# Optimization experiments

Hardware: AMD Instinct MI355X
Metric: run time of the kernel (lower is better)

Reference implementation:

```python
import jax, jax.numpy as jnp
import numpy as np

EMB, HEAD = 2048, 128

def setup_inputs() -> dict:
    key = jax.random.key(0)
    ks = jax.random.split(key, 7)
    x = jax.random.normal(ks[0], (4, 4096, EMB), dtype=jnp.float32)
    s = 1.0 / np.sqrt(EMB)
    wK = jax.random.normal(ks[1], (EMB, HEAD), dtype=jnp.float32) * s
    bK = jax.random.normal(ks[2], (HEAD,), dtype=jnp.float32) * 0.01
    wQ = jax.random.normal(ks[3], (EMB, HEAD), dtype=jnp.float32) * s
    bQ = jax.random.normal(ks[4], (HEAD,), dtype=jnp.float32) * 0.01
    wV = jax.random.normal(ks[5], (EMB, HEAD), dtype=jnp.float32) * s
    bV = jax.random.normal(ks[6], (HEAD,), dtype=jnp.float32) * 0.01
    return {"x": x, "wK": wK, "bK": bK, "wQ": wQ, "bQ": bQ, "wV": wV, "bV": bV}

def reference(x, wK, bK, wQ, bQ, wV, bV):
    B, S, E = x.shape
    K = x @ wK + bK                      # [B,S,H]
    Q = x @ wQ + bQ
    V = x @ wV + bV
    scale = 1.0 / jnp.sqrt(jnp.float32(HEAD))
    att = jnp.einsum('bqh,bkh->bqk', Q, K) * scale   # [B,S,S]
    causal = jnp.tril(jnp.ones((S, S), dtype=bool))
    att = jnp.where(causal, att, -jnp.inf)
    att = jax.nn.softmax(att, axis=-1)
    return jnp.einsum('bqk,bkh->bqh', att, V)        # [B,S,H]
```

## Files before the change

### kernel.cpp

```cpp
#include <hip/hip_runtime.h>
#include <hip/hip_bf16.h>
#include <math.h>

#define SEQ  4096
#define BATCH 4
#define EMBD 2048
#define HDIM 128

#define SCALE_LOG2E 0.12753102721944556f

typedef __bf16 bf16x8 __attribute__((ext_vector_type(8)));
typedef __bf16 bf16x4 __attribute__((ext_vector_type(4)));
typedef float  f32x4  __attribute__((ext_vector_type(4)));

__device__ __forceinline__ bf16x8 ldfrag(const __bf16* p) {
    return *(const bf16x8*)p;
}

__device__ __forceinline__ void gl_lds16(const __bf16* g, __bf16* l) {
    __builtin_amdgcn_global_load_lds(
        (const __attribute__((address_space(1))) void*)g,
        (__attribute__((address_space(3))) void*)l, 16, 0, 0);
}

__global__ __launch_bounds__(256)
void cvt_x(const float* __restrict__ x, __bf16* __restrict__ xb) {
    size_t idx = (size_t)(blockIdx.x * 256 + threadIdx.x) * 8;
    float4 v0 = *(const float4*)(x + idx);
    float4 v1 = *(const float4*)(x + idx + 4);
    bf16x8 o = { (__bf16)v0.x, (__bf16)v0.y, (__bf16)v0.z, (__bf16)v0.w,
                 (__bf16)v1.x, (__bf16)v1.y, (__bf16)v1.z, (__bf16)v1.w };
    *(bf16x8*)(xb + idx) = o;
}

__global__ __launch_bounds__(256)
void cvt_w(const float* __restrict__ wQ, const float* __restrict__ wK,
           const float* __restrict__ wV, __bf16* __restrict__ wt) {
    const float* w = (blockIdx.z == 0) ? wQ : (blockIdx.z == 1) ? wK : wV;
    __bf16* dst = wt + (size_t)blockIdx.z * HDIM * EMBD;
    int k0 = blockIdx.x * 32;
    int n0 = blockIdx.y * 32;
    __shared__ float t[32][33];
    {
        int r  = threadIdx.x >> 3;
        int c4 = (threadIdx.x & 7) * 4;
        float4 v = *(const float4*)(w + (size_t)(k0 + r) * HDIM + n0 + c4);
        t[r][c4 + 0] = v.x; t[r][c4 + 1] = v.y;
        t[r][c4 + 2] = v.z; t[r][c4 + 3] = v.w;
    }
    __syncthreads();
    {
        int n  = threadIdx.x >> 3;
        int k4 = (threadIdx.x & 7) * 4;
        bf16x4 o = { (__bf16)t[k4 + 0][n], (__bf16)t[k4 + 1][n],
                     (__bf16)t[k4 + 2][n], (__bf16)t[k4 + 3][n] };
        *(bf16x4*)(dst + (size_t)(n0 + n) * EMBD + k0 + k4) = o;
    }
}

__global__ __launch_bounds__(256, 3)
void proj(const __bf16* __restrict__ xb,
          const __bf16* __restrict__ wt,
          __bf16* __restrict__ pout) {
    const int mat  = blockIdx.y;
    const int z    = blockIdx.z;
    const int m0   = blockIdx.x * 128;
    const int kb   = z * (EMBD / 2);
    const int wv   = threadIdx.x >> 6;
    const int lane = threadIdx.x & 63;
    const int ln   = lane & 15;
    const int quad = lane >> 4;
    const int r8   = lane >> 3;
    const int c8   = lane & 7;

    __shared__ __bf16 lA[128 * 64];
    __shared__ __bf16 lB[128 * 64];

    const __bf16* wtm = wt + (size_t)mat * (HDIM * EMBD);
    const __bf16* gaS = xb  + (size_t)(m0 + wv * 32 + r8) * EMBD + kb + (c8 ^ r8) * 8;
    const __bf16* gbS = wtm + (size_t)(wv * 32 + r8) * EMBD + kb + (c8 ^ r8) * 8;
    __bf16* laD = lA + (wv * 32) * 64;
    __bf16* lbD = lB + (wv * 32) * 64;

    const int wm0 = (wv >> 1) * 64;
    const int wn0 = (wv & 1) * 64;

    const f32x4 fzero = {0.f, 0.f, 0.f, 0.f};
    f32x4 acc[4][4];
#pragma unroll
    for (int i = 0; i < 4; i++)
#pragma unroll
        for (int j = 0; j < 4; j++) acc[i][j] = fzero;

    for (int k0 = 0; k0 < EMBD / 2; k0 += 64) {
#pragma unroll
        for (int i = 0; i < 4; i++) {
            gl_lds16(gaS + (size_t)i * 8 * EMBD + k0, laD + i * 8 * 64);
            gl_lds16(gbS + (size_t)i * 8 * EMBD + k0, lbD + i * 8 * 64);
        }
        __syncthreads();
#pragma unroll
        for (int kk = 0; kk < 2; kk++) {
            bf16x8 a[4], bb[4];
#pragma unroll
            for (int i = 0; i < 4; i++)
                a[i] = ldfrag(lA + (wm0 + i * 16 + ln) * 64 +
                              (((quad + 4 * kk) ^ (ln & 7)) * 8));
#pragma unroll
            for (int j = 0; j < 4; j++)
                bb[j] = ldfrag(lB + (wn0 + j * 16 + ln) * 64 +
                               (((quad + 4 * kk) ^ (ln & 7)) * 8));
#pragma unroll
            for (int i = 0; i < 4; i++)
#pragma unroll
                for (int j = 0; j < 4; j++)
                    acc[i][j] = __builtin_amdgcn_mfma_f32_16x16x32_bf16(
                        a[i], bb[j], acc[i][j], 0, 0, 0);
        }
        __syncthreads();
    }

    __bf16* pp = pout + (size_t)(mat * 2 + z) * 16384 * 128;
#pragma unroll
    for (int j = 0; j < 4; j++) {
        int col = wn0 + j * 16 + ln;
#pragma unroll
        for (int i = 0; i < 4; i++) {
            int rowb = m0 + wm0 + i * 16 + quad * 4;
#pragma unroll
            for (int r = 0; r < 4; r++)
                pp[(size_t)(rowb + r) * 128 + col] = (__bf16)acc[i][j][r];
        }
    }
}

__global__ __launch_bounds__(256)
void qkv_fin(const __bf16* __restrict__ pout,
             const float* __restrict__ bQ, const float* __restrict__ bK,
             const float* __restrict__ bV,
             __bf16* __restrict__ qws, __bf16* __restrict__ kws,
             __bf16* __restrict__ vtws) {
    const int mat = blockIdx.y;
    const int r0  = blockIdx.x * 16;
    const int t   = threadIdx.x;
    const int rl  = t >> 4;
    const int cc  = (t & 15) * 8;
    const float* bias = (mat == 0) ? bQ : (mat == 1) ? bK : bV;

    bf16x8 p0 = *(const bf16x8*)(pout +
        ((size_t)(mat * 2 + 0) * 16384 + r0 + rl) * 128 + cc);
    bf16x8 p1 = *(const bf16x8*)(pout +
        ((size_t)(mat * 2 + 1) * 16384 + r0 + rl) * 128 + cc);
    float s[8];
#pragma unroll
    for (int i = 0; i < 8; i++)
        s[i] = (float)p0[i] + (float)p1[i] + bias[cc + i];

    if (mat < 2) {
        __bf16* dst = (mat == 0) ? qws : kws;
        bf16x8 o;
#pragma unroll
        for (int i = 0; i < 8; i++) o[i] = (__bf16)s[i];
        *(bf16x8*)(dst + (size_t)(r0 + rl) * 128 + cc) = o;
    } else {
        __shared__ float sm[16][132];
#pragma unroll
        for (int i = 0; i < 8; i++) sm[rl][cc + i] = s[i];
        __syncthreads();
        int col = t >> 1, sg = (t & 1) * 8;
        int bb = r0 >> 12, s0 = r0 & (SEQ - 1);
        bf16x8 o;
#pragma unroll
        for (int i = 0; i < 8; i++) o[i] = (__bf16)sm[sg + i][col];
        *(bf16x8*)(vtws + ((size_t)bb * HDIM + col) * SEQ + s0 + sg) = o;
    }
}

__global__ __launch_bounds__(256, 2)
void attn(const __bf16* __restrict__ qws, const __bf16* __restrict__ kws,
          const __bf16* __restrict__ vtws,
          float* __restrict__ Opart, float* __restrict__ Lpart) {
    const int blk = blockIdx.x;
    const int b   = (blk & 7) >> 1;
    int wi = ((blk >> 3) << 1) | (blk & 1);
    wi = 287 - wi;
    int a = (int)((sqrtf((float)wi + 1.0f) - 1.0f) * 0.5f);
    while (4 * (a + 1) * (a + 2) <= wi) a++;
    while (a > 0 && 4 * a * (a + 1) > wi) a--;
    const int rem = wi - 4 * a * (a + 1);
    const int qt  = a * 8 + rem / (a + 1);
    const int c   = rem - (rem / (a + 1)) * (a + 1);
    const int q0  = qt * 64;
    const int kt0 = c * 8;
    const int kt1 = (kt0 + 8 < qt + 1) ? (kt0 + 8) : (qt + 1);
    const int slot = b * 288 + wi;

    const int wv   = threadIdx.x >> 6;
    const int lane = threadIdx.x & 63;
    const int ln   = lane & 15;
    const int quad = lane >> 4;

    __shared__ __bf16 lK[2][64 * 128];
    __shared__ __bf16 lV[2][128 * 64];
    __shared__ __bf16 lP[4][16 * 72];

    const __bf16* kws_b = kws + (size_t)b * SEQ * HDIM;
    const __bf16* vt_b  = vtws + (size_t)b * HDIM * SEQ;

    const __bf16* qbase =
        qws + ((size_t)(b * SEQ) + q0 + wv * 16 + ln) * HDIM + quad * 8;
    bf16x8 qf[4];
#pragma unroll
    for (int kk = 0; kk < 4; kk++) qf[kk] = ldfrag(qbase + kk * 32);

    const f32x4 fzero = {0.f, 0.f, 0.f, 0.f};
    float lrun[4];
    f32x4 oacc[8];
#pragma unroll
    for (int r = 0; r < 4; r++) lrun[r] = 0.f;
#pragma unroll
    for (int j = 0; j < 8; j++) oacc[j] = fzero;

    const int krow_i = lane >> 4, kslot = lane & 15;
    const int vrow_i = lane >> 3, vslot = lane & 7;

    auto stageK = [&](int k0, int buf) {
#pragma unroll
        for (int i = 0; i < 4; i++) {
            int row = wv * 16 + i * 4 + krow_i;
            const __bf16* src = kws_b + (size_t)(k0 + row) * HDIM +
                                ((kslot ^ (row & 7)) * 8);
            gl_lds16(src, &lK[buf][(wv * 16 + i * 4) * 128]);
        }
    };
    auto stageV = [&](int k0, int buf) {
#pragma unroll
        for (int i = 0; i < 4; i++) {
            int row = wv * 32 + i * 8 + vrow_i;
            const __bf16* src = vt_b + (size_t)row * SEQ + k0 +
                                ((vslot ^ (row & 7)) * 8);
            gl_lds16(src, &lV[buf][(wv * 32 + i * 8) * 64]);
        }
    };

    stageK(kt0 * 64, 0);
    stageV(kt0 * 64, 0);

    for (int kt = kt0; kt < kt1; kt++) {
        __syncthreads();
        const int cur = (kt - kt0) & 1;
        if (kt + 1 < kt1) {
            stageK((kt + 1) * 64, cur ^ 1);
            stageV((kt + 1) * 64, cur ^ 1);
        }

        f32x4 sacc[4];
#pragma unroll
        for (int j = 0; j < 4; j++) sacc[j] = fzero;
        const __bf16* Kb = lK[cur];
#pragma unroll
        for (int j = 0; j < 4; j++) {
#pragma unroll
            for (int kk = 0; kk < 4; kk++) {
                bf16x8 kf = ldfrag(Kb + (j * 16 + ln) * 128 +
                                   (((quad + 4 * kk) ^ (ln & 7)) * 8));
                sacc[j] = __builtin_amdgcn_mfma_f32_16x16x32_bf16(
                    qf[kk], kf, sacc[j], 0, 0, 0);
            }
        }

        const bool diag = (kt == qt);
#pragma unroll
        for (int j = 0; j < 4; j++) {
#pragma unroll
            for (int r = 0; r < 4; r++) {
                float p = exp2f(sacc[j][r] * SCALE_LOG2E);
                if (diag) {
                    int col = kt * 64 + j * 16 + ln;
                    int row = q0 + wv * 16 + quad * 4 + r;
                    if (col > row) p = 0.f;
                }
                lrun[r] += p;
                lP[wv][(quad * 4 + r) * 72 + j * 16 + ln] = (__bf16)p;
            }
        }

        __builtin_amdgcn_s_waitcnt(0xc07f);
        bf16x8 af0 = ldfrag(&lP[wv][ln * 72 + quad * 8]);
        bf16x8 af1 = ldfrag(&lP[wv][ln * 72 + 32 + quad * 8]);

        const __bf16* Vb = lV[cur];
#pragma unroll
        for (int j = 0; j < 8; j++) {
            bf16x8 v0 = ldfrag(Vb + (j * 16 + ln) * 64 +
                               ((quad ^ (ln & 7)) * 8));
            bf16x8 v1 = ldfrag(Vb + (j * 16 + ln) * 64 +
                               (((quad + 4) ^ (ln & 7)) * 8));
            oacc[j] = __builtin_amdgcn_mfma_f32_16x16x32_bf16(
                af0, v0, oacc[j], 0, 0, 0);
            oacc[j] = __builtin_amdgcn_mfma_f32_16x16x32_bf16(
                af1, v1, oacc[j], 0, 0, 0);
        }
    }

#pragma unroll
    for (int r = 0; r < 4; r++) {
#pragma unroll
        for (int off = 8; off >= 1; off >>= 1)
            lrun[r] += __shfl_xor(lrun[r], off);
    }
    if (ln == 0) {
#pragma unroll
        for (int r = 0; r < 4; r++)
            Lpart[(size_t)slot * 64 + wv * 16 + quad * 4 + r] = lrun[r];
    }
    float* Ob = Opart + (size_t)slot * 8192;
#pragma unroll
    for (int r = 0; r < 4; r++) {
        int row = wv * 16 + quad * 4 + r;
#pragma unroll
        for (int j = 0; j < 8; j++)
            Ob[(size_t)row * 128 + j * 16 + ln] = oacc[j][r];
    }
}

__global__ __launch_bounds__(256)
void attn_fin(const float* __restrict__ Opart, const float* __restrict__ Lpart,
              float* __restrict__ out) {
    const int b  = blockIdx.x >> 6;
    const int qt = blockIdx.x & 63;
    const int a  = qt >> 3;
    const int nch = a + 1;
    const int base = b * 288 + 4 * a * (a + 1) + (qt & 7) * (a + 1);
    const int row = threadIdx.x >> 2;
    const int c0  = (threadIdx.x & 3) * 32;

    float l = 0.f;
    f32x4 o[8];
#pragma unroll
    for (int i = 0; i < 8; i++) o[i] = {0.f, 0.f, 0.f, 0.f};
    for (int ch = 0; ch < nch; ch++) {
        const f32x4* Op = (const f32x4*)(Opart + (size_t)(base + ch) * 8192 +
                                         (size_t)row * 128 + c0);
        l += Lpart[(size_t)(base + ch) * 64 + row];
#pragma unroll
        for (int i = 0; i < 8; i++) o[i] += Op[i];
    }
    float inv = 1.f / l;
    f32x4* orow = (f32x4*)(out + ((size_t)(b * SEQ) + qt * 64 + row) * HDIM + c0);
#pragma unroll
    for (int i = 0; i < 8; i++) orow[i] = o[i] * inv;
}

extern "C" void kernel_launch(void* const* d_in, const int* in_sizes, int n_in,
                              void* d_out, int out_size, void* d_ws,
                              size_t ws_size, hipStream_t stream) {
    const float* x  = (const float*)d_in[0];
    const float* wK = (const float*)d_in[1];
    const float* bK = (const float*)d_in[2];
    const float* wQ = (const float*)d_in[3];
    const float* bQ = (const float*)d_in[4];
    const float* wV = (const float*)d_in[5];
    const float* bV = (const float*)d_in[6];
    float* out = (float*)d_out;

    __bf16* xb   = (__bf16*)d_ws;
    __bf16* wt   = xb + (size_t)BATCH * SEQ * EMBD;
    __bf16* qws  = wt + (size_t)3 * HDIM * EMBD;
    __bf16* kws  = qws + (size_t)BATCH * SEQ * HDIM;
    __bf16* vtws = kws + (size_t)BATCH * SEQ * HDIM;
    __bf16* pout = vtws + (size_t)BATCH * SEQ * HDIM;
    float* Opart = (float*)d_ws;
    float* Lpart = Opart + (size_t)1152 * 8192;

    hipLaunchKernelGGL(cvt_w, dim3(EMBD / 32, HDIM / 32, 3), dim3(256), 0,
                       stream, wQ, wK, wV, wt);
    hipLaunchKernelGGL(cvt_x, dim3((size_t)BATCH * SEQ * EMBD / (8 * 256)),
                       dim3(256), 0, stream, x, xb);
    hipLaunchKernelGGL(proj, dim3(SEQ * BATCH / 128, 3, 2), dim3(256), 0,
                       stream, xb, wt, pout);
    hipLaunchKernelGGL(qkv_fin, dim3(SEQ * BATCH / 16, 3), dim3(256), 0,
                       stream, pout, bQ, bK, bV, qws, kws, vtws);
    hipLaunchKernelGGL(attn, dim3(1152), dim3(256), 0, stream,
                       qws, kws, vtws, Opart, Lpart);
    hipLaunchKernelGGL(attn_fin, dim3(256), dim3(256), 0, stream,
                       Opart, Lpart, out);
}
```

Measured before the change: 307.8 us.

## Switch to 32x32x16 MFMA and enlarge attention query tiles to 128 rows

Replaces the 16x16x32 MFMA tiles in the projection and attention kernels with 32x32x16 MFMA, which gives each wave a 32-row tile and more reuse per fragment load. The attention work split moves from 64-row query tiles in 8-key-tile chunks (1152 blocks) to 128-row query tiles in 16-key-tile chunks (320 blocks). Half the waves are skipped on the last diagonal key tile. Larger accumulators raise register pressure. Far fewer blocks may underfill the GPU, and the partial-sum workspace layout changes to match.

```diff
diff --git a/kernel.cpp b/kernel.cpp
--- a/kernel.cpp
+++ b/kernel.cpp
@@ -1,6 +1,5 @@
 #include <hip/hip_runtime.h>
 #include <hip/hip_bf16.h>
-#include <math.h>
 
 #define SEQ  4096
 #define BATCH 4
@@ -12,6 +11,7 @@
 typedef __bf16 bf16x8 __attribute__((ext_vector_type(8)));
 typedef __bf16 bf16x4 __attribute__((ext_vector_type(4)));
 typedef float  f32x4  __attribute__((ext_vector_type(4)));
+typedef float  f32x16 __attribute__((ext_vector_type(16)));
 
 __device__ __forceinline__ bf16x8 ldfrag(const __bf16* p) {
     return *(const bf16x8*)p;
@@ -68,8 +68,8 @@
     const int kb   = z * (EMBD / 2);
     const int wv   = threadIdx.x >> 6;
     const int lane = threadIdx.x & 63;
-    const int ln   = lane & 15;
-    const int quad = lane >> 4;
+    const int l31  = lane & 31;
+    const int h    = lane >> 5;
     const int r8   = lane >> 3;
     const int c8   = lane & 7;
 
@@ -85,12 +85,13 @@
     const int wm0 = (wv >> 1) * 64;
     const int wn0 = (wv & 1) * 64;
 
-    const f32x4 fzero = {0.f, 0.f, 0.f, 0.f};
-    f32x4 acc[4][4];
-#pragma unroll
-    for (int i = 0; i < 4; i++)
-#pragma unroll
-        for (int j = 0; j < 4; j++) acc[i][j] = fzero;
+    f32x16 acc[2][2];
+#pragma unroll
+    for (int i = 0; i < 2; i++)
+#pragma unroll
+        for (int j = 0; j < 2; j++)
+#pragma unroll
+            for (int e = 0; e < 16; e++) acc[i][j][e] = 0.f;
 
     for (int k0 = 0; k0 < EMBD / 2; k0 += 64) {
 #pragma unroll
@@ -100,21 +101,24 @@
         }
         __syncthreads();
 #pragma unroll
-        for (int kk = 0; kk < 2; kk++) {
-            bf16x8 a[4], bb[4];
-#pragma unroll
-            for (int i = 0; i < 4; i++)
-                a[i] = ldfrag(lA + (wm0 + i * 16 + ln) * 64 +
-                              (((quad + 4 * kk) ^ (ln & 7)) * 8));
-#pragma unroll
-            for (int j = 0; j < 4; j++)
-                bb[j] = ldfrag(lB + (wn0 + j * 16 + ln) * 64 +
-                               (((quad + 4 * kk) ^ (ln & 7)) * 8));
-#pragma unroll
-            for (int i = 0; i < 4; i++)
-#pragma unroll
-                for (int j = 0; j < 4; j++)
-                    acc[i][j] = __builtin_amdgcn_mfma_f32_16x16x32_bf16(
+        for (int kk = 0; kk < 4; kk++) {
+            const int ch = kk * 2 + h;
+            bf16x8 a[2], bb[2];
+#pragma unroll
+            for (int i = 0; i < 2; i++) {
+                int row = wm0 + i * 32 + l31;
+                a[i] = ldfrag(lA + row * 64 + ((ch ^ (row & 7)) * 8));
+            }
+#pragma unroll
+            for (int j = 0; j < 2; j++) {
+                int row = wn0 + j * 32 + l31;
+                bb[j] = ldfrag(lB + row * 64 + ((ch ^ (row & 7)) * 8));
+            }
+#pragma unroll
+            for (int i = 0; i < 2; i++)
+#pragma unroll
+                for (int j = 0; j < 2; j++)
+                    acc[i][j] = __builtin_amdgcn_mfma_f32_32x32x16_bf16(
                         a[i], bb[j], acc[i][j], 0, 0, 0);
         }
         __syncthreads();
@@ -122,16 +126,16 @@
 
     __bf16* pp = pout + (size_t)(mat * 2 + z) * 16384 * 128;
 #pragma unroll
-    for (int j = 0; j < 4; j++) {
-        int col = wn0 + j * 16 + ln;
-#pragma unroll
-        for (int i = 0; i < 4; i++) {
-            int rowb = m0 + wm0 + i * 16 + quad * 4;
-#pragma unroll
-            for (int r = 0; r < 4; r++)
-                pp[(size_t)(rowb + r) * 128 + col] = (__bf16)acc[i][j][r];
-        }
-    }
+    for (int i = 0; i < 2; i++)
+#pragma unroll
+        for (int j = 0; j < 2; j++) {
+            int n = wn0 + j * 32 + l31;
+#pragma unroll
+            for (int reg = 0; reg < 16; reg++) {
+                int m = m0 + wm0 + i * 32 + (reg & 3) + 8 * (reg >> 2) + 4 * h;
+                pp[(size_t)m * 128 + n] = (__bf16)acc[i][j][reg];
+            }
+        }
 }
 
 __global__ __launch_bounds__(256)
@@ -176,50 +180,50 @@
     }
 }
 
-__global__ __launch_bounds__(256, 2)
+__global__ __launch_bounds__(256)
 void attn(const __bf16* __restrict__ qws, const __bf16* __restrict__ kws,
           const __bf16* __restrict__ vtws,
           float* __restrict__ Opart, float* __restrict__ Lpart) {
     const int blk = blockIdx.x;
     const int b   = (blk & 7) >> 1;
     int wi = ((blk >> 3) << 1) | (blk & 1);
-    wi = 287 - wi;
-    int a = (int)((sqrtf((float)wi + 1.0f) - 1.0f) * 0.5f);
-    while (4 * (a + 1) * (a + 2) <= wi) a++;
-    while (a > 0 && 4 * a * (a + 1) > wi) a--;
+    wi = 79 - wi;
+    const int a   = (wi < 8) ? 0 : (wi < 24) ? 1 : (wi < 48) ? 2 : 3;
     const int rem = wi - 4 * a * (a + 1);
     const int qt  = a * 8 + rem / (a + 1);
     const int c   = rem - (rem / (a + 1)) * (a + 1);
-    const int q0  = qt * 64;
-    const int kt0 = c * 8;
-    const int kt1 = (kt0 + 8 < qt + 1) ? (kt0 + 8) : (qt + 1);
-    const int slot = b * 288 + wi;
+    const int q0  = qt * 128;
+    const int kt0 = c * 16;
+    const int ktN = 2 * qt + 2;
+    const int kt1 = (kt0 + 16 < ktN) ? (kt0 + 16) : ktN;
+    const int slot = b * 80 + wi;
 
     const int wv   = threadIdx.x >> 6;
     const int lane = threadIdx.x & 63;
-    const int ln   = lane & 15;
-    const int quad = lane >> 4;
-
-    __shared__ __bf16 lK[2][64 * 128];
-    __shared__ __bf16 lV[2][128 * 64];
-    __shared__ __bf16 lP[4][16 * 72];
+    const int l31  = lane & 31;
+    const int h    = lane >> 5;
+
+    __shared__ __align__(16) __bf16 lK[2][64 * 128];
+    __shared__ __align__(16) __bf16 lV[2][128 * 64];
+    __shared__ __align__(16) __bf16 lP[4][32 * 72];
 
     const __bf16* kws_b = kws + (size_t)b * SEQ * HDIM;
     const __bf16* vt_b  = vtws + (size_t)b * HDIM * SEQ;
 
     const __bf16* qbase =
-        qws + ((size_t)(b * SEQ) + q0 + wv * 16 + ln) * HDIM + quad * 8;
-    bf16x8 qf[4];
-#pragma unroll
-    for (int kk = 0; kk < 4; kk++) qf[kk] = ldfrag(qbase + kk * 32);
-
-    const f32x4 fzero = {0.f, 0.f, 0.f, 0.f};
-    float lrun[4];
-    f32x4 oacc[8];
-#pragma unroll
-    for (int r = 0; r < 4; r++) lrun[r] = 0.f;
-#pragma unroll
-    for (int j = 0; j < 8; j++) oacc[j] = fzero;
+        qws + ((size_t)(b * SEQ) + q0 + wv * 32 + l31) * HDIM + h * 8;
+    bf16x8 qf[8];
+#pragma unroll
+    for (int ks = 0; ks < 8; ks++) qf[ks] = ldfrag(qbase + ks * 16);
+
+    float lrun[16];
+#pragma unroll
+    for (int e = 0; e < 16; e++) lrun[e] = 0.f;
+    f32x16 oacc[4];
+#pragma unroll
+    for (int jj = 0; jj < 4; jj++)
+#pragma unroll
+        for (int e = 0; e < 16; e++) oacc[jj][e] = 0.f;
 
     const int krow_i = lane >> 4, kslot = lane & 15;
     const int vrow_i = lane >> 3, vslot = lane & 7;
@@ -254,102 +258,113 @@
             stageV((kt + 1) * 64, cur ^ 1);
         }
 
-        f32x4 sacc[4];
-#pragma unroll
-        for (int j = 0; j < 4; j++) sacc[j] = fzero;
-        const __bf16* Kb = lK[cur];
-#pragma unroll
-        for (int j = 0; j < 4; j++) {
-#pragma unroll
-            for (int kk = 0; kk < 4; kk++) {
-                bf16x8 kf = ldfrag(Kb + (j * 16 + ln) * 128 +
-                                   (((quad + 4 * kk) ^ (ln & 7)) * 8));
-                sacc[j] = __builtin_amdgcn_mfma_f32_16x16x32_bf16(
-                    qf[kk], kf, sacc[j], 0, 0, 0);
-            }
-        }
-
-        const bool diag = (kt == qt);
-#pragma unroll
-        for (int j = 0; j < 4; j++) {
-#pragma unroll
-            for (int r = 0; r < 4; r++) {
-                float p = exp2f(sacc[j][r] * SCALE_LOG2E);
-                if (diag) {
-                    int col = kt * 64 + j * 16 + ln;
-                    int row = q0 + wv * 16 + quad * 4 + r;
-                    if (col > row) p = 0.f;
+        const bool active = !(kt == 2 * qt + 1 && wv < 2);
+        if (active) {
+            f32x16 sacc[2];
+#pragma unroll
+            for (int j = 0; j < 2; j++)
+#pragma unroll
+                for (int e = 0; e < 16; e++) sacc[j][e] = 0.f;
+            const __bf16* Kb = lK[cur];
+#pragma unroll
+            for (int ks = 0; ks < 8; ks++) {
+                const int c16 = ks * 2 + h;
+#pragma unroll
+                for (int j = 0; j < 2; j++) {
+                    int row = j * 32 + l31;
+                    bf16x8 kf = ldfrag(Kb + row * 128 +
+                                       ((c16 ^ (row & 7)) * 8));
+                    sacc[j] = __builtin_amdgcn_mfma_f32_32x32x16_bf16(
+                        qf[ks], kf, sacc[j], 0, 0, 0);
                 }
-                lrun[r] += p;
-                lP[wv][(quad * 4 + r) * 72 + j * 16 + ln] = (__bf16)p;
-            }
-        }
-
-        __builtin_amdgcn_s_waitcnt(0xc07f);
-        bf16x8 af0 = ldfrag(&lP[wv][ln * 72 + quad * 8]);
-        bf16x8 af1 = ldfrag(&lP[wv][ln * 72 + 32 + quad * 8]);
-
-        const __bf16* Vb = lV[cur];
-#pragma unroll
-        for (int j = 0; j < 8; j++) {
-            bf16x8 v0 = ldfrag(Vb + (j * 16 + ln) * 64 +
-                               ((quad ^ (ln & 7)) * 8));
-            bf16x8 v1 = ldfrag(Vb + (j * 16 + ln) * 64 +
-                               (((quad + 4) ^ (ln & 7)) * 8));
-            oacc[j] = __builtin_amdgcn_mfma_f32_16x16x32_bf16(
-                af0, v0, oacc[j], 0, 0, 0);
-            oacc[j] = __builtin_amdgcn_mfma_f32_16x16x32_bf16(
-                af1, v1, oacc[j], 0, 0, 0);
-        }
-    }
-
-#pragma unroll
-    for (int r = 0; r < 4; r++) {
-#pragma unroll
-        for (int off = 8; off >= 1; off >>= 1)
-            lrun[r] += __shfl_xor(lrun[r], off);
-    }
-    if (ln == 0) {
-#pragma unroll
-        for (int r = 0; r < 4; r++)
-            Lpart[(size_t)slot * 64 + wv * 16 + quad * 4 + r] = lrun[r];
-    }
-    float* Ob = Opart + (size_t)slot * 8192;
-#pragma unroll
-    for (int r = 0; r < 4; r++) {
-        int row = wv * 16 + quad * 4 + r;
-#pragma unroll
-        for (int j = 0; j < 8; j++)
-            Ob[(size_t)row * 128 + j * 16 + ln] = oacc[j][r];
+            }
+
+            const bool maskt = (kt >= 2 * qt);
+#pragma unroll
+            for (int j = 0; j < 2; j++) {
+#pragma unroll
+                for (int reg = 0; reg < 16; reg++) {
+                    int rl = (reg & 3) + 8 * (reg >> 2) + 4 * h;
+                    float p = exp2f(sacc[j][reg] * SCALE_LOG2E);
+                    if (maskt) {
+                        int col = kt * 64 + j * 32 + l31;
+                        int row = q0 + wv * 32 + rl;
+                        if (col > row) p = 0.f;
+                    }
+                    lrun[reg] += (j == 0) ? p : p;
+                    lP[wv][rl * 72 + j * 32 + l31] = (__bf16)p;
+                }
+            }
+
+            __builtin_amdgcn_s_waitcnt(0xc07f);
+            const __bf16* Vb = lV[cur];
+#pragma unroll
+            for (int ks2 = 0; ks2 < 4; ks2++) {
+                bf16x8 af = ldfrag(&lP[wv][l31 * 72 + ks2 * 16 + h * 8]);
+                const int ch = ks2 * 2 + h;
+#pragma unroll
+                for (int jj = 0; jj < 4; jj++) {
+                    int row = jj * 32 + l31;
+                    bf16x8 vf = ldfrag(Vb + row * 64 +
+                                       ((ch ^ (row & 7)) * 8));
+                    oacc[jj] = __builtin_amdgcn_mfma_f32_32x32x16_bf16(
+                        af, vf, oacc[jj], 0, 0, 0);
+                }
+            }
+        }
+    }
+
+#pragma unroll
+    for (int reg = 0; reg < 16; reg++) {
+#pragma unroll
+        for (int off = 16; off >= 1; off >>= 1)
+            lrun[reg] += __shfl_xor(lrun[reg], off);
+    }
+    if (l31 == 0) {
+#pragma unroll
+        for (int reg = 0; reg < 16; reg++) {
+            int row = wv * 32 + (reg & 3) + 8 * (reg >> 2) + 4 * h;
+            Lpart[(size_t)slot * 128 + row] = lrun[reg];
+        }
+    }
+    float* Ob = Opart + (size_t)slot * 16384;
+#pragma unroll
+    for (int jj = 0; jj < 4; jj++) {
+        int col = jj * 32 + l31;
+#pragma unroll
+        for (int reg = 0; reg < 16; reg++) {
+            int row = wv * 32 + (reg & 3) + 8 * (reg >> 2) + 4 * h;
+            Ob[(size_t)row * 128 + col] = oacc[jj][reg];
+        }
     }
 }
 
 __global__ __launch_bounds__(256)
 void attn_fin(const float* __restrict__ Opart, const float* __restrict__ Lpart,
               float* __restrict__ out) {
-    const int b  = blockIdx.x >> 6;
-    const int qt = blockIdx.x & 63;
+    const int b  = blockIdx.x >> 5;
+    const int qt = blockIdx.x & 31;
     const int a  = qt >> 3;
     const int nch = a + 1;
-    const int base = b * 288 + 4 * a * (a + 1) + (qt & 7) * (a + 1);
-    const int row = threadIdx.x >> 2;
-    const int c0  = (threadIdx.x & 3) * 32;
+    const int base = b * 80 + 4 * a * (a + 1) + (qt & 7) * (a + 1);
+    const int row = threadIdx.x >> 1;
+    const int c0  = (threadIdx.x & 1) * 64;
 
     float l = 0.f;
-    f32x4 o[8];
-#pragma unroll
-    for (int i = 0; i < 8; i++) o[i] = {0.f, 0.f, 0.f, 0.f};
+    f32x4 o[16];
+#pragma unroll
+    for (int i = 0; i < 16; i++) o[i] = {0.f, 0.f, 0.f, 0.f};
     for (int ch = 0; ch < nch; ch++) {
-        const f32x4* Op = (const f32x4*)(Opart + (size_t)(base + ch) * 8192 +
+        const f32x4* Op = (const f32x4*)(Opart + (size_t)(base + ch) * 16384 +
                                          (size_t)row * 128 + c0);
-        l += Lpart[(size_t)(base + ch) * 64 + row];
-#pragma unroll
-        for (int i = 0; i < 8; i++) o[i] += Op[i];
+        l += Lpart[(size_t)(base + ch) * 128 + row];
+#pragma unroll
+        for (int i = 0; i < 16; i++) o[i] += Op[i];
     }
     float inv = 1.f / l;
-    f32x4* orow = (f32x4*)(out + ((size_t)(b * SEQ) + qt * 64 + row) * HDIM + c0);
-#pragma unroll
-    for (int i = 0; i < 8; i++) orow[i] = o[i] * inv;
+    f32x4* orow = (f32x4*)(out + ((size_t)(b * SEQ) + qt * 128 + row) * HDIM + c0);
+#pragma unroll
+    for (int i = 0; i < 16; i++) orow[i] = o[i] * inv;
 }
 
 extern "C" void kernel_launch(void* const* d_in, const int* in_sizes, int n_in,
@@ -371,7 +386,7 @@
     __bf16* vtws = kws + (size_t)BATCH * SEQ * HDIM;
     __bf16* pout = vtws + (size_t)BATCH * SEQ * HDIM;
     float* Opart = (float*)d_ws;
-    float* Lpart = Opart + (size_t)1152 * 8192;
+    float* Lpart = Opart + (size_t)320 * 16384;
 
     hipLaunchKernelGGL(cvt_w, dim3(EMBD / 32, HDIM / 32, 3), dim3(256), 0,
                        stream, wQ, wK, wV, wt);
@@ -381,8 +396,8 @@
                        stream, xb, wt, pout);
     hipLaunchKernelGGL(qkv_fin, dim3(SEQ * BATCH / 16, 3), dim3(256), 0,
                        stream, pout, bQ, bK, bV, qws, kws, vtws);
-    hipLaunchKernelGGL(attn, dim3(1152), dim3(256), 0, stream,
+    hipLaunchKernelGGL(attn, dim3(320), dim3(256), 0, stream,
                        qws, kws, vtws, Opart, Lpart);
-    hipLaunchKernelGGL(attn_fin, dim3(256), dim3(256), 0, stream,
+    hipLaunchKernelGGL(attn_fin, dim3(128), dim3(256), 0, stream,
                        Opart, Lpart, out);
 }
```

Result: slower. 348.2 us (+13.1%).
